# Kernel optimization log

Hardware: AMD Instinct MI355X
Metric: run time of the kernel (lower is better)

## Reference

```python
import jax, jax.numpy as jnp
import numpy as np

N = 30000      # total atoms in batch
E = 60000      # directed bonds
FIN = 64       # raw atom feature dim (in_channels)
H = 768        # hidden_channels
G = 600        # number of graphs
L = 20         # seq_length
NL = 3         # num_layers
EA = 6         # edge_attr dim (hard-coded: Linear(in_channels + 6, ...))
EPS = 1e-5     # BatchNorm eps


def _bn(x, g, b, m, v):
    # eval-mode BatchNorm1d with running stats
    return (x - m) * jax.lax.rsqrt(v + EPS) * g + b


def setup_inputs() -> dict:
    key = jax.random.key(0)
    ks = list(jax.random.split(key, 48))
    kit = iter(ks)

    def rn(shp, s=0.02):
        return jax.random.normal(next(kit), shp, jnp.float32) * s

    def bn_params(shape_prefix=()):
        g = jax.random.uniform(next(kit), shape_prefix + (H,), jnp.float32, 0.5, 1.5)
        b = rn(shape_prefix + (H,), 0.1)
        m = rn(shape_prefix + (H,), 0.1)
        v = jax.random.uniform(next(kit), shape_prefix + (H,), jnp.float32, 0.5, 1.5)
        return g, b, m, v

    inp = {}
    inp["x"] = jax.random.normal(next(kit), (N, FIN), jnp.float32)
    inp["edge_index"] = jax.random.randint(next(kit), (2, E), 0, N)
    inp["edge_attr"] = jax.random.uniform(next(kit), (E, EA), jnp.float32)
    inp["batch_idx"] = jnp.sort(jax.random.randint(next(kit), (N,), 0, G))
    inp["num_graphs"] = G

    # input_mlp
    inp["W_in"] = rn((FIN, H)); inp["b_in"] = rn((H,))
    inp["bn0_g"], inp["bn0_b"], inp["bn0_m"], inp["bn0_v"] = bn_params()
    # stacked WLNConv layers
    inp["Wc"] = rn((NL, H + EA, H)); inp["bc"] = rn((NL, H))
    inp["bnc_g"], inp["bnc_b"], inp["bnc_m"], inp["bnc_v"] = bn_params((NL,))
    # sequence_proj
    inp["Ws"] = rn((3 * H, H)); inp["bs"] = rn((H,))
    inp["bns_g"], inp["bns_b"], inp["bns_m"], inp["bns_v"] = bn_params()
    # pooler
    inp["Wp"] = rn((H, H)); inp["bp"] = rn((H,))
    # node_decoder
    inp["Wd1"] = rn((H, H)); inp["bd1"] = rn((H,))
    inp["bnd_g"], inp["bnd_b"], inp["bnd_m"], inp["bnd_v"] = bn_params()
    inp["Wd2"] = rn((H, FIN)); inp["bd2"] = rn((FIN,))
    return inp


def reference(x, edge_index, edge_attr, batch_idx, num_graphs,
              W_in, b_in, bn0_g, bn0_b, bn0_m, bn0_v,
              Wc, bc, bnc_g, bnc_b, bnc_m, bnc_v,
              Ws, bs, bns_g, bns_b, bns_m, bns_v,
              Wp, bp,
              Wd1, bd1, bnd_g, bnd_b, bnd_m, bnd_v,
              Wd2, bd2):
    n = x.shape[0]
    # input_mlp (eval: dropout = identity)
    h = _bn(jnp.maximum(x @ W_in + b_in, 0.0), bn0_g, bn0_b, bn0_m, bn0_v)

    # add self loops once (same edge list for every conv layer)
    loops = jnp.arange(n)
    src = jnp.concatenate([edge_index[0], loops])            # [E+N]
    dst = jnp.concatenate([edge_index[1], loops])            # [E+N]
    ea = jnp.concatenate(
        [edge_attr, jnp.zeros((n, edge_attr.shape[1]), edge_attr.dtype)], axis=0)

    total = h
    for i in range(Wc.shape[0]):
        # message: gather x_j, concat edge_attr, linear + relu
        m_in = jnp.concatenate([h[src], ea], axis=1)          # [E+N, H+6]
        msg = jnp.maximum(m_in @ Wc[i] + bc[i], 0.0)          # [E+N, H]
        # aggregate: scatter-add into target nodes
        agg = jax.ops.segment_sum(msg, dst, num_segments=n)   # [N, H]
        h = _bn(agg, bnc_g[i], bnc_b[i], bnc_m[i], bnc_v[i])
        total = total + h                                     # sum over layer outputs

    # global pools per graph
    counts = jax.ops.segment_sum(jnp.ones((n,), total.dtype), batch_idx,
                                 num_segments=num_graphs)     # [G]
    x_add = jax.ops.segment_sum(total, batch_idx, num_segments=num_graphs)
    x_mean = x_add / jnp.maximum(counts, 1.0)[:, None]
    x_max = jax.ops.segment_max(total, batch_idx, num_segments=num_graphs)
    x_max = jnp.where(counts[:, None] > 0, x_max, 0.0)

    comb = jnp.concatenate([x_mean, x_add, x_max], axis=1)    # [G, 3H]
    hs = _bn(jnp.maximum(comb @ Ws + bs, 0.0), bns_g, bns_b, bns_m, bns_v)

    last_hidden = jnp.broadcast_to(hs[:, None, :], (hs.shape[0], L, hs.shape[1]))
    pooler = jnp.tanh(hs @ Wp + bp)                           # [G, H]

    # expand graph embedding back to nodes (batch_idx is sorted -> gather)
    z = pooler[batch_idx]                                     # [N, H]
    d = _bn(jnp.maximum(z @ Wd1 + bd1, 0.0), bnd_g, bnd_b, bnd_m, bnd_v)
    recon = d @ Wd2 + bd2                                     # [N, FIN]
    return last_hidden, pooler, recon
```

## Files before the change

### kernel.cpp

```cpp
#include <hip/hip_runtime.h>

#define NATOMS 30000
#define NPAD   30080
#define NEDGE  60000
#define HDIM   768
#define H4     192
#define NG     600
#define GPAD   640
#define LSEQ   20
#define BNEPS  1e-5f

typedef __attribute__((ext_vector_type(8))) short bf16x8;
typedef __attribute__((ext_vector_type(4))) float f32x4;

__device__ __forceinline__ ushort f2bf(float f) {
    union { float f; unsigned u; } v; v.f = f;
    unsigned r = v.u + 0x7FFFu + ((v.u >> 16) & 1u);
    return (ushort)(r >> 16);
}
__device__ __forceinline__ float bf2f(ushort u) {
    union { unsigned u; float f; } v; v.u = ((unsigned)u) << 16; return v.f;
}
__device__ __forceinline__ ushort4 pack4(float4 v) {
    ushort4 r; r.x = f2bf(v.x); r.y = f2bf(v.y); r.z = f2bf(v.z); r.w = f2bf(v.w); return r;
}
__device__ __forceinline__ float4 unpack4(ushort4 u) {
    float4 r; r.x = bf2f(u.x); r.y = bf2f(u.y); r.z = bf2f(u.z); r.w = bf2f(u.w); return r;
}
__device__ __forceinline__ void gl_lds16(const ushort* g, ushort* l) {
    __builtin_amdgcn_global_load_lds(
        (const __attribute__((address_space(1))) void*)(g),
        (__attribute__((address_space(3))) void*)(l), 16, 0, 0);
}

#define PC0 (3L*768*768)
#define PC1 (PC0 + 768L*64)
#define PC2 (PC1 + 768L*2304)
#define PC3 (PC2 + 768L*768)
#define PC4 (PC3 + 768L*768)
#define PC5 (PC4 + 128L*768)
#define PC6 (PC5 + 480000L)
#define PC7 (PC6 + NATOMS)
__global__ __launch_bounds__(256) void prep_k(
    const float* __restrict__ Wc, const float* __restrict__ Win, const float* __restrict__ Ws,
    const float* __restrict__ Wp, const float* __restrict__ Wd1, const float* __restrict__ Wd2,
    const float* __restrict__ x,
    ushort* __restrict__ WTc, ushort* __restrict__ WinT, ushort* __restrict__ WsT,
    ushort* __restrict__ WpT, ushort* __restrict__ Wd1T, ushort* __restrict__ Wd2T,
    ushort* __restrict__ XB, int* __restrict__ cnt)
{
    long idx = (long)blockIdx.x * 256 + threadIdx.x;
    if (idx < PC0) {
        long b = idx / (768 * 768), rem = idx % (768 * 768);
        long n = rem / 768, k = rem % 768;
        WTc[idx] = f2bf(Wc[b * 594432 + k * 768 + n]);
    } else if (idx < PC1) {
        long j = idx - PC0; long n = j / 64, k = j % 64;
        WinT[j] = f2bf(Win[k * 768 + n]);
    } else if (idx < PC2) {
        long j = idx - PC1; long n = j / 2304, k = j % 2304;
        WsT[j] = f2bf(Ws[k * 768 + n]);
    } else if (idx < PC3) {
        long j = idx - PC2; long n = j / 768, k = j % 768;
        WpT[j] = f2bf(Wp[k * 768 + n]);
    } else if (idx < PC4) {
        long j = idx - PC3; long n = j / 768, k = j % 768;
        Wd1T[j] = f2bf(Wd1[k * 768 + n]);
    } else if (idx < PC5) {
        long j = idx - PC4; long n = j / 768, k = j % 768;
        Wd2T[j] = (n < 64) ? f2bf(Wd2[k * 64 + n]) : (ushort)0;
    } else if (idx < PC6) {
        long j = idx - PC5;
        ((ushort4*)XB)[j] = pack4(((const float4*)x)[j]);
    } else if (idx < PC7) {
        cnt[idx - PC6] = 0;
    }
}

template <int EPI, int SWZ>
__global__ __launch_bounds__(256) void gemm_bt(
    const ushort* __restrict__ A, const ushort* __restrict__ Bt,
    float* __restrict__ Cf, ushort* __restrict__ Cb, ushort* __restrict__ Cb2,
    const float* __restrict__ bias,
    const float* __restrict__ bng, const float* __restrict__ bnb,
    const float* __restrict__ bnm, const float* __restrict__ bnv,
    int Mreal, int Nreal, int K, int nbx)
{
    __shared__ ushort As[2][128 * 32];
    __shared__ ushort Bs[2][128 * 32];
    int t = threadIdx.x;
    int lane = t & 63, wave = t >> 6;
    int wr = wave >> 1, wc = wave & 1;
    int brow, bcol;
    if (SWZ) {
        int nwg = gridDim.x;
        int q = nwg >> 3, r = nwg & 7;
        int id = blockIdx.x;
        int xcd = id & 7, i = id >> 3;
        int s = (xcd < r) ? xcd * (q + 1) + i : r * (q + 1) + (xcd - r) * q + i;
        bcol = s % 6; brow = s / 6;
    } else {
        bcol = blockIdx.x; brow = blockIdx.y;
    }

    f32x4 acc[4][4];
    #pragma unroll
    for (int i = 0; i < 4; i++)
        #pragma unroll
        for (int j = 0; j < 4; j++) acc[i][j] = (f32x4)0.f;

    const int r0 = wave * 32 + (lane >> 2);
    const int ce = (lane & 3) * 8;
    const ushort* Ag0 = A + (size_t)(brow * 128 + r0) * K + ce;
    const ushort* Ag1 = A + (size_t)(brow * 128 + r0 + 16) * K + ce;
    const ushort* Bg0 = Bt + (size_t)(bcol * 128 + r0) * K + ce;
    const ushort* Bg1 = Bt + (size_t)(bcol * 128 + r0 + 16) * K + ce;
    const int wo = wave * 1024;

    const int lr = lane & 15, lk = (lane >> 4) * 8;

    gl_lds16(Ag0, &As[0][wo]);
    gl_lds16(Ag1, &As[0][wo + 512]);
    gl_lds16(Bg0, &Bs[0][wo]);
    gl_lds16(Bg1, &Bs[0][wo + 512]);
    __syncthreads();

    int cur = 0;
    for (int kt = 0; kt < K; kt += 32) {
        if (kt + 32 < K) {
            int nb = cur ^ 1;
            gl_lds16(Ag0 + kt + 32, &As[nb][wo]);
            gl_lds16(Ag1 + kt + 32, &As[nb][wo + 512]);
            gl_lds16(Bg0 + kt + 32, &Bs[nb][wo]);
            gl_lds16(Bg1 + kt + 32, &Bs[nb][wo + 512]);
        }

        bf16x8 af[4], bfr[4];
        #pragma unroll
        for (int mf = 0; mf < 4; mf++)
            af[mf] = *(const bf16x8*)(&As[cur][(wr * 64 + mf * 16 + lr) * 32 + lk]);
        #pragma unroll
        for (int nf = 0; nf < 4; nf++)
            bfr[nf] = *(const bf16x8*)(&Bs[cur][(wc * 64 + nf * 16 + lr) * 32 + lk]);
        #pragma unroll
        for (int mf = 0; mf < 4; mf++)
            #pragma unroll
            for (int nf = 0; nf < 4; nf++)
                acc[mf][nf] = __builtin_amdgcn_mfma_f32_16x16x32_bf16(af[mf], bfr[nf], acc[mf][nf], 0, 0, 0);

        __syncthreads();
        cur ^= 1;
    }

    const int lq = lane >> 4;
    #pragma unroll
    for (int mf = 0; mf < 4; mf++) {
        #pragma unroll
        for (int nf = 0; nf < 4; nf++) {
            int col = bcol * 128 + wc * 64 + nf * 16 + lr;
            #pragma unroll
            for (int rg = 0; rg < 4; rg++) {
                int row = brow * 128 + wr * 64 + mf * 16 + lq * 4 + rg;
                if (row < Mreal && col < Nreal) {
                    float v = acc[mf][nf][rg];
                    if (EPI >= 1) v += bias[col];
                    if (EPI == 1) {
                        v = fmaxf(v, 0.f);
                        float s = bng[col] * rsqrtf(bnv[col] + BNEPS);
                        v = (v - bnm[col]) * s + bnb[col];
                    } else if (EPI == 2) {
                        v = tanhf(v);
                    }
                    size_t o = (size_t)row * Nreal + col;
                    if (Cf) Cf[o] = v;
                    if (Cb) Cb[o] = f2bf(v);
                    if (Cb2) Cb2[o] = f2bf(v);
                }
            }
        }
    }
}


__global__ void count_k(const int* __restrict__ dst_a, int* __restrict__ cnt)
{
    int e = blockIdx.x * 256 + threadIdx.x;
    if (e < NEDGE) atomicAdd(&cnt[dst_a[e]], 1);
}

__global__ __launch_bounds__(1024) void scan_k(const int* __restrict__ cnt,
                                               int* __restrict__ row_off,
                                               int* __restrict__ cur)
{
    __shared__ int part[1024];
    const int CH = (NATOMS + 1023) / 1024;
    int t = threadIdx.x;
    int base = t * CH;
    int s = 0;
    for (int i = base; i < base + CH && i < NATOMS; i++) s += cnt[i];
    part[t] = s;
    __syncthreads();
    for (int off = 1; off < 1024; off <<= 1) {
        int v = (t >= off) ? part[t - off] : 0;
        __syncthreads();
        part[t] += v;
        __syncthreads();
    }
    int excl = part[t] - s;
    for (int i = base; i < base + CH && i < NATOMS; i++) {
        row_off[i] = excl;
        cur[i] = excl;
        excl += cnt[i];
    }
    if (t == 1023) row_off[NATOMS] = part[1023];
}

__global__ void fill_k(const int* __restrict__ src_a, const int* __restrict__ dst_a,
                       const float* __restrict__ ea,
                       int* __restrict__ cur, int* __restrict__ srcs, float* __restrict__ eas)
{
    int e = blockIdx.x * 256 + threadIdx.x;
    if (e >= NEDGE) return;
    int d = dst_a[e];
    int pos = atomicAdd(&cur[d], 1);
    srcs[pos] = src_a[e];
    float* o = eas + (size_t)pos * 8;
    o[0] = ea[e * 6 + 0]; o[1] = ea[e * 6 + 1]; o[2] = ea[e * 6 + 2];
    o[3] = ea[e * 6 + 3]; o[4] = ea[e * 6 + 4]; o[5] = ea[e * 6 + 5];
}

#define NPN 8
__global__ __launch_bounds__(192) void node_agg_k(
    const ushort* __restrict__ P, const int* __restrict__ row_off,
    const int* __restrict__ srcs, const float* __restrict__ eas,
    const float* __restrict__ Wce, const float* __restrict__ bc,
    const float* __restrict__ g, const float* __restrict__ b,
    const float* __restrict__ m, const float* __restrict__ vv,
    ushort* __restrict__ TOTAL, ushort* __restrict__ HB)
{
    int n0 = blockIdx.x * NPN;
    int c4 = threadIdx.x;
    const float4* W4 = (const float4*)Wce;
    float4 w0 = W4[0 * H4 + c4], w1 = W4[1 * H4 + c4], w2 = W4[2 * H4 + c4];
    float4 w3 = W4[3 * H4 + c4], w4 = W4[4 * H4 + c4], w5 = W4[5 * H4 + c4];
    float4 bb = ((const float4*)bc)[c4];
    float4 gg = ((const float4*)g)[c4], bo = ((const float4*)b)[c4];
    float4 mm = ((const float4*)m)[c4], vq = ((const float4*)vv)[c4];
    float4 sc;
    sc.x = gg.x * rsqrtf(vq.x + BNEPS); sc.y = gg.y * rsqrtf(vq.y + BNEPS);
    sc.z = gg.z * rsqrtf(vq.z + BNEPS); sc.w = gg.w * rsqrtf(vq.w + BNEPS);

    for (int u = 0; u < NPN; u++) {
        int n = n0 + u;
        if (n >= NATOMS) return;
        float4 p = unpack4(((const ushort4*)P)[(size_t)n * H4 + c4]);
        float4 acc;
        acc.x = fmaxf(p.x + bb.x, 0.f); acc.y = fmaxf(p.y + bb.y, 0.f);
        acc.z = fmaxf(p.z + bb.z, 0.f); acc.w = fmaxf(p.w + bb.w, 0.f);

        int lo = row_off[n], hi = row_off[n + 1];
        for (int j = lo; j < hi; j++) {
            int s = srcs[j];
            const float* e8 = eas + (size_t)j * 8;
            float4 eA = *(const float4*)(e8);
            float e4v = e8[4], e5v = e8[5];
            float4 ps = unpack4(((const ushort4*)P)[(size_t)s * H4 + c4]);
            float4 v;
            v.x = fmaxf(ps.x + eA.x * w0.x + eA.y * w1.x + eA.z * w2.x + eA.w * w3.x + e4v * w4.x + e5v * w5.x + bb.x, 0.f);
            v.y = fmaxf(ps.y + eA.x * w0.y + eA.y * w1.y + eA.z * w2.y + eA.w * w3.y + e4v * w4.y + e5v * w5.y + bb.y, 0.f);
            v.z = fmaxf(ps.z + eA.x * w0.z + eA.y * w1.z + eA.z * w2.z + eA.w * w3.z + e4v * w4.z + e5v * w5.z + bb.z, 0.f);
            v.w = fmaxf(ps.w + eA.x * w0.w + eA.y * w1.w + eA.z * w2.w + eA.w * w3.w + e4v * w4.w + e5v * w5.w + bb.w, 0.f);
            acc.x += v.x; acc.y += v.y; acc.z += v.z; acc.w += v.w;
        }

        float4 hv;
        hv.x = (acc.x - mm.x) * sc.x + bo.x;
        hv.y = (acc.y - mm.y) * sc.y + bo.y;
        hv.z = (acc.z - mm.z) * sc.z + bo.z;
        hv.w = (acc.w - mm.w) * sc.w + bo.w;
        size_t idx = (size_t)n * H4 + c4;
        float4 tt = unpack4(((const ushort4*)TOTAL)[idx]);
        tt.x += hv.x; tt.y += hv.y; tt.z += hv.z; tt.w += hv.w;
        ((ushort4*)TOTAL)[idx] = pack4(tt);
        ((ushort4*)HB)[idx] = pack4(hv);
    }
}

__global__ __launch_bounds__(64) void pool_k(const ushort* __restrict__ TOTAL,
                                             const int* __restrict__ bidx,
                                             ushort* __restrict__ COMB)
{
    int g = blockIdx.x;
    int c4 = blockIdx.y * 64 + threadIdx.x;
    ushort4* C4 = (ushort4*)COMB;
    int lo, hi;
    { int a = 0, b = NATOMS; while (a < b) { int mid = (a + b) >> 1; if (bidx[mid] < g) a = mid + 1; else b = mid; } lo = a; }
    { int a = lo, b = NATOMS; while (a < b) { int mid = (a + b) >> 1; if (bidx[mid] <= g) a = mid + 1; else b = mid; } hi = a; }
    int cnt = hi - lo;
    float4 sum = {0.f, 0.f, 0.f, 0.f};
    float4 mx = {-INFINITY, -INFINITY, -INFINITY, -INFINITY};
    for (int r = lo; r < hi; r++) {
        float4 v = unpack4(((const ushort4*)TOTAL)[(size_t)r * H4 + c4]);
        sum.x += v.x; sum.y += v.y; sum.z += v.z; sum.w += v.w;
        mx.x = fmaxf(mx.x, v.x); mx.y = fmaxf(mx.y, v.y);
        mx.z = fmaxf(mx.z, v.z); mx.w = fmaxf(mx.w, v.w);
    }
    float inv = 1.f / fmaxf((float)cnt, 1.f);
    if (cnt == 0) { mx.x = mx.y = mx.z = mx.w = 0.f; }
    float4 mean = {sum.x * inv, sum.y * inv, sum.z * inv, sum.w * inv};
    C4[(size_t)g * 576 + c4] = pack4(mean);
    C4[(size_t)g * 576 + 192 + c4] = pack4(sum);
    C4[(size_t)g * 576 + 384 + c4] = pack4(mx);
}

__global__ void bcast_k(const float* __restrict__ HS, float* __restrict__ out0)
{
    size_t idx = (size_t)blockIdx.x * 256 + threadIdx.x;
    int c4 = (int)(idx % H4);
    int g = (int)(idx / ((size_t)H4 * LSEQ));
    ((float4*)out0)[idx] = ((const float4*)HS)[(size_t)g * H4 + c4];
}

__global__ void recon_k(const float* __restrict__ RG, const int* __restrict__ bidx,
                        float* __restrict__ out2)
{
    size_t idx = (size_t)blockIdx.x * 256 + threadIdx.x;
    int n = (int)(idx >> 4), c4 = (int)(idx & 15);
    ((float4*)out2)[idx] = ((const float4*)RG)[(size_t)bidx[n] * 16 + c4];
}

extern "C" void kernel_launch(void* const* d_in, const int* in_sizes, int n_in,
                              void* d_out, int out_size, void* d_ws, size_t ws_size,
                              hipStream_t stream)
{
    const float* x    = (const float*)d_in[0];
    const int*   ei   = (const int*)d_in[1];
    const float* ea   = (const float*)d_in[2];
    const int*   bidx = (const int*)d_in[3];
    const float* Win  = (const float*)d_in[5];
    const float* bin  = (const float*)d_in[6];
    const float* bn0g = (const float*)d_in[7];
    const float* bn0b = (const float*)d_in[8];
    const float* bn0m = (const float*)d_in[9];
    const float* bn0v = (const float*)d_in[10];
    const float* Wc   = (const float*)d_in[11];
    const float* bc   = (const float*)d_in[12];
    const float* bncg = (const float*)d_in[13];
    const float* bncb = (const float*)d_in[14];
    const float* bncm = (const float*)d_in[15];
    const float* bncv = (const float*)d_in[16];
    const float* Ws   = (const float*)d_in[17];
    const float* bs   = (const float*)d_in[18];
    const float* bnsg = (const float*)d_in[19];
    const float* bnsb = (const float*)d_in[20];
    const float* bnsm = (const float*)d_in[21];
    const float* bnsv = (const float*)d_in[22];
    const float* Wp   = (const float*)d_in[23];
    const float* bp   = (const float*)d_in[24];
    const float* Wd1  = (const float*)d_in[25];
    const float* bd1  = (const float*)d_in[26];
    const float* bndg = (const float*)d_in[27];
    const float* bndb = (const float*)d_in[28];
    const float* bndm = (const float*)d_in[29];
    const float* bndv = (const float*)d_in[30];
    const float* Wd2  = (const float*)d_in[31];
    const float* bd2  = (const float*)d_in[32];

    float* out  = (float*)d_out;
    float* out0 = out;
    float* out1 = out + (size_t)NG * LSEQ * HDIM;
    float* out2 = out1 + (size_t)NG * HDIM;

    char* w = (char*)d_ws;
    size_t off = 0;
    auto alloc = [&](size_t bytes) { void* p = w + off; off += (bytes + 255) & ~255ULL; return p; };
    ushort* P      = (ushort*)alloc((size_t)NPAD * HDIM * 2);
    ushort* TOTAL  = (ushort*)alloc((size_t)NATOMS * HDIM * 2);
    ushort* HB     = (ushort*)alloc((size_t)NPAD * HDIM * 2);
    ushort* XB     = (ushort*)alloc((size_t)NPAD * 64 * 2);
    ushort* WTc    = (ushort*)alloc((size_t)3 * 768 * 768 * 2);
    ushort* WinT   = (ushort*)alloc((size_t)768 * 64 * 2);
    ushort* WsT    = (ushort*)alloc((size_t)768 * 2304 * 2);
    ushort* WpT    = (ushort*)alloc((size_t)768 * 768 * 2);
    ushort* Wd1T   = (ushort*)alloc((size_t)768 * 768 * 2);
    ushort* Wd2T   = (ushort*)alloc((size_t)128 * 768 * 2);
    ushort* COMB   = (ushort*)alloc((size_t)GPAD * 2304 * 2);
    float*  HS     = (float*) alloc((size_t)NG * HDIM * 4);
    ushort* HSB    = (ushort*)alloc((size_t)GPAD * HDIM * 2);
    ushort* POOLB  = (ushort*)alloc((size_t)GPAD * HDIM * 2);
    ushort* DGB    = (ushort*)alloc((size_t)GPAD * HDIM * 2);
    float*  RECONG = (float*) alloc((size_t)NG * 64 * 4);
    int*    cnt    = (int*)   alloc((size_t)NATOMS * 4);
    int*    row_off= (int*)   alloc((size_t)(NATOMS + 1) * 4);
    int*    cur    = (int*)   alloc((size_t)NATOMS * 4);
    int*    srcs   = (int*)   alloc((size_t)NEDGE * 4);
    float*  eas    = (float*) alloc((size_t)NEDGE * 8 * 4);

    const int* src_a = ei;
    const int* dst_a = ei + NEDGE;

    prep_k<<<(int)((PC7 + 255) / 256), 256, 0, stream>>>(
        Wc, Win, Ws, Wp, Wd1, Wd2, x, WTc, WinT, WsT, WpT, Wd1T, Wd2T, XB, cnt);

    count_k<<<(NEDGE + 255) / 256, 256, 0, stream>>>(dst_a, cnt);
    scan_k<<<1, 1024, 0, stream>>>(cnt, row_off, cur);
    fill_k<<<(NEDGE + 255) / 256, 256, 0, stream>>>(src_a, dst_a, ea, cur, srcs, eas);

    gemm_bt<1, 1><<<1410, 256, 0, stream>>>(
        XB, WinT, nullptr, HB, TOTAL, bin, bn0g, bn0b, bn0m, bn0v, NATOMS, HDIM, 64, 6);

    for (int i = 0; i < 3; i++) {
        const float* Wcei = Wc + (size_t)i * 774 * HDIM + (size_t)HDIM * HDIM;
        const float* bci  = bc + i * HDIM;
        gemm_bt<0, 1><<<1410, 256, 0, stream>>>(
            HB, WTc + (size_t)i * 768 * 768, nullptr, P, nullptr,
            nullptr, nullptr, nullptr, nullptr, nullptr, NATOMS, HDIM, HDIM, 6);
        node_agg_k<<<(NATOMS + NPN - 1) / NPN, 192, 0, stream>>>(
            P, row_off, srcs, eas, Wcei, bci,
            bncg + i * HDIM, bncb + i * HDIM, bncm + i * HDIM, bncv + i * HDIM, TOTAL, HB);
    }

    pool_k<<<dim3(NG, 3), 64, 0, stream>>>(TOTAL, bidx, COMB);

    gemm_bt<1, 0><<<dim3(6, 5), 256, 0, stream>>>(
        COMB, WsT, HS, HSB, nullptr, bs, bnsg, bnsb, bnsm, bnsv, NG, HDIM, 2304, 6);

    bcast_k<<<(NG * LSEQ * H4) / 256, 256, 0, stream>>>(HS, out0);

    gemm_bt<2, 0><<<dim3(6, 5), 256, 0, stream>>>(
        HSB, WpT, out1, POOLB, nullptr, bp, nullptr, nullptr, nullptr, nullptr, NG, HDIM, HDIM, 6);

    gemm_bt<1, 0><<<dim3(6, 5), 256, 0, stream>>>(
        POOLB, Wd1T, nullptr, DGB, nullptr, bd1, bndg, bndb, bndm, bndv, NG, HDIM, HDIM, 6);

    gemm_bt<3, 0><<<dim3(1, 5), 256, 0, stream>>>(
        DGB, Wd2T, RECONG, nullptr, nullptr, bd2, nullptr, nullptr, nullptr, nullptr, NG, 64, HDIM, 1);

    recon_k<<<(NATOMS * 16) / 256, 256, 0, stream>>>(RECONG, bidx, out2);
}
```

Measured before the change: 771.7 us.

## Split-K the small graph-level GEMMs with a separate reduction epilogue

New measurement: 668.1 us. 1.16x faster.

```diff
diff --git a/kernel.cpp b/kernel.cpp
--- a/kernel.cpp
+++ b/kernel.cpp
@@ -9,6 +9,7 @@
 #define GPAD   640
 #define LSEQ   20
 #define BNEPS  1e-5f
+#define KS     8
 
 typedef __attribute__((ext_vector_type(8))) short bf16x8;
 typedef __attribute__((ext_vector_type(4))) float f32x4;
@@ -178,6 +179,119 @@
                 }
             }
         }
+    }
+}
+
+__global__ __launch_bounds__(256) void gemm_pk(
+    const ushort* __restrict__ A, const ushort* __restrict__ Bt,
+    float* __restrict__ CP, int Nstr, int K)
+{
+    __shared__ ushort As[2][128 * 32];
+    __shared__ ushort Bs[2][128 * 32];
+    int t = threadIdx.x;
+    int lane = t & 63, wave = t >> 6;
+    int wr = wave >> 1, wc = wave & 1;
+    int bcol = blockIdx.x, brow = blockIdx.y, ks = blockIdx.z;
+    const int KL = K / KS;
+    const int k0 = ks * KL, k1 = k0 + KL;
+
+    f32x4 acc[4][4];
+    #pragma unroll
+    for (int i = 0; i < 4; i++)
+        #pragma unroll
+        for (int j = 0; j < 4; j++) acc[i][j] = (f32x4)0.f;
+
+    const int r0 = wave * 32 + (lane >> 2);
+    const int ce = (lane & 3) * 8;
+    const ushort* Ag0 = A + (size_t)(brow * 128 + r0) * K + ce;
+    const ushort* Ag1 = A + (size_t)(brow * 128 + r0 + 16) * K + ce;
+    const ushort* Bg0 = Bt + (size_t)(bcol * 128 + r0) * K + ce;
+    const ushort* Bg1 = Bt + (size_t)(bcol * 128 + r0 + 16) * K + ce;
+    const int wo = wave * 1024;
+    const int lr = lane & 15, lk = (lane >> 4) * 8;
+
+    gl_lds16(Ag0 + k0, &As[0][wo]);
+    gl_lds16(Ag1 + k0, &As[0][wo + 512]);
+    gl_lds16(Bg0 + k0, &Bs[0][wo]);
+    gl_lds16(Bg1 + k0, &Bs[0][wo + 512]);
+    __syncthreads();
+
+    int cur = 0;
+    for (int kt = k0; kt < k1; kt += 32) {
+        if (kt + 32 < k1) {
+            int nb = cur ^ 1;
+            gl_lds16(Ag0 + kt + 32, &As[nb][wo]);
+            gl_lds16(Ag1 + kt + 32, &As[nb][wo + 512]);
+            gl_lds16(Bg0 + kt + 32, &Bs[nb][wo]);
+            gl_lds16(Bg1 + kt + 32, &Bs[nb][wo + 512]);
+        }
+        bf16x8 af[4], bfr[4];
+        #pragma unroll
+        for (int mf = 0; mf < 4; mf++)
+            af[mf] = *(const bf16x8*)(&As[cur][(wr * 64 + mf * 16 + lr) * 32 + lk]);
+        #pragma unroll
+        for (int nf = 0; nf < 4; nf++)
+            bfr[nf] = *(const bf16x8*)(&Bs[cur][(wc * 64 + nf * 16 + lr) * 32 + lk]);
+        #pragma unroll
+        for (int mf = 0; mf < 4; mf++)
+            #pragma unroll
+            for (int nf = 0; nf < 4; nf++)
+                acc[mf][nf] = __builtin_amdgcn_mfma_f32_16x16x32_bf16(af[mf], bfr[nf], acc[mf][nf], 0, 0, 0);
+        __syncthreads();
+        cur ^= 1;
+    }
+
+    const int lq = lane >> 4;
+    float* cp = CP + (size_t)ks * 640 * Nstr;
+    #pragma unroll
+    for (int mf = 0; mf < 4; mf++) {
+        #pragma unroll
+        for (int nf = 0; nf < 4; nf++) {
+            int col = bcol * 128 + wc * 64 + nf * 16 + lr;
+            #pragma unroll
+            for (int rg = 0; rg < 4; rg++) {
+                int row = brow * 128 + wr * 64 + mf * 16 + lq * 4 + rg;
+                cp[(size_t)row * Nstr + col] = acc[mf][nf][rg];
+            }
+        }
+    }
+}
+
+template <int EPI>
+__global__ __launch_bounds__(256) void epi_k(
+    const float* __restrict__ CP, int Nstr, int Nreal, int outStride,
+    float* __restrict__ Cf, ushort* __restrict__ Cb,
+    const float* __restrict__ bias,
+    const float* __restrict__ bng, const float* __restrict__ bnb,
+    const float* __restrict__ bnm, const float* __restrict__ bnv)
+{
+    int idx = blockIdx.x * 256 + threadIdx.x;
+    int n4 = Nstr >> 2;
+    int row = idx / n4, c4 = idx - row * n4;
+    if (row >= NG) return;
+    int col = c4 * 4;
+    float4 s = {0.f, 0.f, 0.f, 0.f};
+    #pragma unroll
+    for (int ks = 0; ks < KS; ks++) {
+        float4 p = *(const float4*)(CP + (size_t)ks * 640 * Nstr + (size_t)row * Nstr + col);
+        s.x += p.x; s.y += p.y; s.z += p.z; s.w += p.w;
+    }
+    float v[4] = {s.x, s.y, s.z, s.w};
+    #pragma unroll
+    for (int j = 0; j < 4; j++) {
+        int c = col + j;
+        if (c >= Nreal) break;
+        float u = v[j] + bias[c];
+        if (EPI == 1) {
+            u = fmaxf(u, 0.f);
+            float sc = bng[c] * rsqrtf(bnv[c] + BNEPS);
+            u = (u - bnm[c]) * sc + bnb[c];
+        } else if (EPI == 2) {
+            u = tanhf(u);
+        }
+        size_t o = (size_t)row * outStride + c;
+        if (Cf) Cf[o] = u;
+        if (Cb) Cb[o] = f2bf(u);
     }
 }
 
@@ -385,6 +499,7 @@
     ushort* Wd1T   = (ushort*)alloc((size_t)768 * 768 * 2);
     ushort* Wd2T   = (ushort*)alloc((size_t)128 * 768 * 2);
     ushort* COMB   = (ushort*)alloc((size_t)GPAD * 2304 * 2);
+    float*  CP     = (float*) alloc((size_t)KS * 640 * 768 * 4);
     float*  HS     = (float*) alloc((size_t)NG * HDIM * 4);
     ushort* HSB    = (ushort*)alloc((size_t)GPAD * HDIM * 2);
     ushort* POOLB  = (ushort*)alloc((size_t)GPAD * HDIM * 2);
@@ -422,19 +537,23 @@
 
     pool_k<<<dim3(NG, 3), 64, 0, stream>>>(TOTAL, bidx, COMB);
 
-    gemm_bt<1, 0><<<dim3(6, 5), 256, 0, stream>>>(
-        COMB, WsT, HS, HSB, nullptr, bs, bnsg, bnsb, bnsm, bnsv, NG, HDIM, 2304, 6);
+    gemm_pk<<<dim3(6, 5, KS), 256, 0, stream>>>(COMB, WsT, CP, 768, 2304);
+    epi_k<1><<<(NG * 192 + 255) / 256, 256, 0, stream>>>(
+        CP, 768, 768, 768, HS, HSB, bs, bnsg, bnsb, bnsm, bnsv);
 
     bcast_k<<<(NG * LSEQ * H4) / 256, 256, 0, stream>>>(HS, out0);
 
-    gemm_bt<2, 0><<<dim3(6, 5), 256, 0, stream>>>(
-        HSB, WpT, out1, POOLB, nullptr, bp, nullptr, nullptr, nullptr, nullptr, NG, HDIM, HDIM, 6);
-
-    gemm_bt<1, 0><<<dim3(6, 5), 256, 0, stream>>>(
-        POOLB, Wd1T, nullptr, DGB, nullptr, bd1, bndg, bndb, bndm, bndv, NG, HDIM, HDIM, 6);
-
-    gemm_bt<3, 0><<<dim3(1, 5), 256, 0, stream>>>(
-        DGB, Wd2T, RECONG, nullptr, nullptr, bd2, nullptr, nullptr, nullptr, nullptr, NG, 64, HDIM, 1);
+    gemm_pk<<<dim3(6, 5, KS), 256, 0, stream>>>(HSB, WpT, CP, 768, 768);
+    epi_k<2><<<(NG * 192 + 255) / 256, 256, 0, stream>>>(
+        CP, 768, 768, 768, out1, POOLB, bp, nullptr, nullptr, nullptr, nullptr);
+
+    gemm_pk<<<dim3(6, 5, KS), 256, 0, stream>>>(POOLB, Wd1T, CP, 768, 768);
+    epi_k<1><<<(NG * 192 + 255) / 256, 256, 0, stream>>>(
+        CP, 768, 768, 768, nullptr, DGB, bd1, bndg, bndb, bndm, bndv);
+
+    gemm_pk<<<dim3(1, 5, KS), 256, 0, stream>>>(DGB, Wd2T, CP, 128, 768);
+    epi_k<3><<<(NG * 32 + 255) / 256, 256, 0, stream>>>(
+        CP, 128, 64, 64, RECONG, nullptr, bd2, nullptr, nullptr, nullptr, nullptr);
 
     recon_k<<<(NATOMS * 16) / 256, 256, 0, stream>>>(RECONG, bidx, out2);
 }
```
